# Kernel optimization log

Measured on AMD Instinct MI355X. Metric: run time of the kernel, lower is better.

## Reference

```python
import jax, jax.numpy as jnp
import numpy as np

B, N, HID = 32768, 27, 128
SINKHORN_ITERS = 20
LN_EPS = 1e-5


def _layer_norm(x, g, b):
    mu = jnp.mean(x, axis=-1, keepdims=True)
    var = jnp.mean((x - mu) ** 2, axis=-1, keepdims=True)
    return (x - mu) * jax.lax.rsqrt(var + LN_EPS) * g + b


def setup_inputs() -> dict:
    key = jax.random.key(0)
    ks = jax.random.split(key, 6)
    A = jax.random.uniform(ks[0], (B, N, N), dtype=jnp.float32)
    m = jax.random.normal(ks[1], (B, N), dtype=jnp.float32)
    tau_r = jnp.ones((), dtype=jnp.float32)
    # MLP params: LayerNorm(4) -> Linear(4,128) -> ReLU -> Linear(128,128) -> LayerNorm(128)
    ln1_g = jnp.ones((4,), jnp.float32)
    ln1_b = jnp.zeros((4,), jnp.float32)
    W1 = jax.random.normal(ks[2], (4, HID), dtype=jnp.float32) * 0.1
    b1 = jnp.zeros((HID,), jnp.float32)
    W2 = jax.random.normal(ks[3], (HID, HID), dtype=jnp.float32) * 0.05
    b2 = jnp.zeros((HID,), jnp.float32)
    ln2_g = jnp.ones((HID,), jnp.float32)
    ln2_b = jnp.zeros((HID,), jnp.float32)
    protos = jax.random.normal(ks[4], (N, HID), dtype=jnp.float32) * 0.02
    return {"A": A, "m": m, "tau_r": tau_r, "ln1_g": ln1_g, "ln1_b": ln1_b,
            "W1": W1, "b1": b1, "W2": W2, "b2": b2,
            "ln2_g": ln2_g, "ln2_b": ln2_b, "protos": protos}


def reference(A, m, tau_r, ln1_g, ln1_b, W1, b1, W2, b2, ln2_g, ln2_b, protos):
    # ---- feature build: [log1p(rowsum), top1_offdiag, top2_offdiag, m] ----
    row_sum = jnp.sum(A, axis=-1)                       # (B,N)
    eye = jnp.eye(N, dtype=A.dtype)
    offdiag = A * (1.0 - eye)                           # (B,N,N)
    top2_vals, _ = jax.lax.top_k(offdiag, 2)            # (B,N,2)
    feat = jnp.stack([jnp.log1p(row_sum), top2_vals[..., 0], top2_vals[..., 1], m], axis=-1)  # (B,N,4)
    # ---- MLP: LN -> Linear -> ReLU -> (Dropout=id) -> Linear -> LN ----
    h = _layer_norm(feat, ln1_g, ln1_b)
    h = jax.nn.relu(h @ W1 + b1)
    h = h @ W2 + b2
    H = _layer_norm(h, ln2_g, ln2_b)                    # (B,N,HID)
    # ---- scores vs slot prototypes, transposed, temperature ----
    scores = jnp.einsum('bnh,kh->bnk', H, protos)       # (B,N,N)
    log_alpha = jnp.swapaxes(scores, 1, 2) / tau_r
    # ---- log-domain Sinkhorn, 20 iterations ----
    def body(_, la):
        la = la - jax.nn.logsumexp(la, axis=-1, keepdims=True)
        la = la - jax.nn.logsumexp(la, axis=-2, keepdims=True)
        return la
    log_alpha = jax.lax.fori_loop(0, SINKHORN_ITERS, body, log_alpha)
    return jnp.exp(log_alpha)                           # (B,N,N) soft permutation R_L
```

## Files before the change

kernel.cpp:

```cpp
#include <hip/hip_runtime.h>
#include <math.h>

#define NN 27
#define HID 128
#define SITERS 20
#define H1S 136

typedef float    v4    __attribute__((ext_vector_type(4)));
typedef _Float16 f16x8 __attribute__((ext_vector_type(8)));

__global__ void k0_prep(const float* __restrict__ W2, const float* __restrict__ protos,
                        _Float16* __restrict__ Bsw, _Float16* __restrict__ Asw)
{
    int t0 = blockIdx.x * 256 + threadIdx.x;
    for (int idx = t0; idx < 4*8*64*8; idx += 8*256) {
        int j = idx & 7, l = (idx >> 3) & 63, nt = (idx >> 9) & 7, kt = idx >> 12;
        int k = kt*32 + (l >> 4)*8 + j, n = nt*16 + (l & 15);
        Bsw[idx] = (_Float16)W2[k*HID + n];
    }
    for (int idx = t0; idx < 2*4*64*8; idx += 8*256) {
        int j = idx & 7, l = (idx >> 3) & 63, kt = (idx >> 9) & 3, mt = idx >> 11;
        int k = kt*32 + (l >> 4)*8 + j, mm = mt*16 + (l & 15);
        Asw[idx] = (mm < NN) ? (_Float16)protos[mm*HID + k] : (_Float16)0.0f;
    }
}

__global__ __launch_bounds__(128, 8) void k1_mlp(
    const float* __restrict__ A, const float* __restrict__ m,
    const float* __restrict__ tau_r,
    const float* __restrict__ ln1g, const float* __restrict__ ln1b,
    const float* __restrict__ W1, const float* __restrict__ b1,
    const float* __restrict__ b2,
    const float* __restrict__ ln2g, const float* __restrict__ ln2b,
    const _Float16* __restrict__ Bsw, const _Float16* __restrict__ Asw,
    float* __restrict__ out)
{
    __shared__ __align__(16) _Float16 sBuf[32 * H1S];
    __shared__ __align__(16) float    sFeat[NN*4 + 4];

    float*    sA  = (float*)sBuf;
    _Float16* sH1 = sBuf;
    _Float16* sH  = sBuf;
    float*    sS  = (float*)sBuf;

    const int b   = blockIdx.x;
    const int tid = threadIdx.x;
    const int l = tid & 63, w = tid >> 6;
    const int c = l & 15, g = l >> 4;
    const float* Ab = A + (size_t)b * (NN * NN);

    for (int i = tid; i < NN * NN; i += 128) sA[i] = Ab[i];
    __syncthreads();

    if (tid < NN) {
        const int n = tid;
        float sum = 0.f, m1 = -1e30f, m2 = -1e30f;
        #pragma unroll
        for (int j = 0; j < NN; ++j) {
            float a = sA[n * NN + j];
            sum += a;
            float v = (j == n) ? 0.f : a;
            float nm1 = fmaxf(m1, v);
            m2 = fmaxf(m2, fminf(m1, v));
            m1 = nm1;
        }
        float f0 = log1pf(sum), f1 = m1, f2 = m2, f3 = m[(size_t)b * NN + n];
        float mu = 0.25f * (f0 + f1 + f2 + f3);
        float d0 = f0 - mu, d1 = f1 - mu, d2 = f2 - mu, d3 = f3 - mu;
        float var = 0.25f * (d0*d0 + d1*d1 + d2*d2 + d3*d3);
        float rs  = rsqrtf(var + 1e-5f);
        sFeat[n*4 + 0] = d0 * rs * ln1g[0] + ln1b[0];
        sFeat[n*4 + 1] = d1 * rs * ln1g[1] + ln1b[1];
        sFeat[n*4 + 2] = d2 * rs * ln1g[2] + ln1b[2];
        sFeat[n*4 + 3] = d3 * rs * ln1g[3] + ln1b[3];
    }
    __syncthreads();

    {
        const float w0 = W1[tid], w1 = W1[HID + tid], w2 = W1[2*HID + tid], w3 = W1[3*HID + tid];
        const float bb = b1[tid];
        #pragma unroll 9
        for (int n = 0; n < NN; ++n) {
            v4 f = *(const v4*)&sFeat[n * 4];
            float v = fmaf(f[0], w0, fmaf(f[1], w1, fmaf(f[2], w2, fmaf(f[3], w3, bb))));
            sH1[n * H1S + tid] = (_Float16)fmaxf(v, 0.f);
        }
        #pragma unroll
        for (int n = NN; n < 32; ++n) sH1[n * H1S + tid] = (_Float16)0.f;
    }
    __syncthreads();

    f16x8 af[4];
    #pragma unroll
    for (int kt = 0; kt < 4; ++kt)
        af[kt] = *(const f16x8*)&sH1[(w*16 + c) * H1S + kt*32 + g*8];

    const f16x8* Bv = (const f16x8*)Bsw;

    float s4[4]  = {0.f, 0.f, 0.f, 0.f};
    float ss4[4] = {0.f, 0.f, 0.f, 0.f};
    #pragma unroll 1
    for (int nt = 0; nt < 8; ++nt) {
        v4 a = (v4)(0.f);
        #pragma unroll
        for (int kt = 0; kt < 4; ++kt)
            a = __builtin_amdgcn_mfma_f32_16x16x32_f16(af[kt], Bv[(kt*8 + nt)*64 + l], a, 0, 0, 0);
        float b2v = b2[nt*16 + c];
        #pragma unroll
        for (int r = 0; r < 4; ++r) {
            float v = a[r] + b2v;
            s4[r] += v; ss4[r] += v * v;
        }
    }
    float muv[4], rsv[4];
    #pragma unroll
    for (int r = 0; r < 4; ++r) {
        #pragma unroll
        for (int mask = 1; mask <= 8; mask <<= 1) {
            s4[r]  += __shfl_xor(s4[r],  mask);
            ss4[r] += __shfl_xor(ss4[r], mask);
        }
        float mu  = s4[r] * (1.0f / HID);
        float var = ss4[r] * (1.0f / HID) - mu * mu;
        muv[r] = mu;
        rsv[r] = rsqrtf(var + 1e-5f);
    }

    #pragma unroll 1
    for (int nt = 0; nt < 8; ++nt) {
        v4 a = (v4)(0.f);
        #pragma unroll
        for (int kt = 0; kt < 4; ++kt)
            a = __builtin_amdgcn_mfma_f32_16x16x32_f16(af[kt], Bv[(kt*8 + nt)*64 + l], a, 0, 0, 0);
        int col = nt*16 + c;
        float b2v = b2[col], g2 = ln2g[col], bb = ln2b[col];
        #pragma unroll
        for (int r = 0; r < 4; ++r) {
            float hv = (a[r] + b2v - muv[r]) * rsv[r] * g2 + bb;
            sH[(w*16 + 4*g + r) * H1S + col] = (_Float16)hv;
        }
    }
    __syncthreads();

    v4 acc2[2];
    {
        const f16x8* Av = (const f16x8*)Asw;
        acc2[0] = (v4)(0.f); acc2[1] = (v4)(0.f);
        #pragma unroll
        for (int kt = 0; kt < 4; ++kt) {
            f16x8 pa  = Av[(w*4 + kt)*64 + l];
            f16x8 b0  = *(const f16x8*)&sH[(c)      * H1S + kt*32 + g*8];
            f16x8 b1f = *(const f16x8*)&sH[(16 + c) * H1S + kt*32 + g*8];
            acc2[0] = __builtin_amdgcn_mfma_f32_16x16x32_f16(pa, b0,  acc2[0], 0, 0, 0);
            acc2[1] = __builtin_amdgcn_mfma_f32_16x16x32_f16(pa, b1f, acc2[1], 0, 0, 0);
        }
    }
    __syncthreads();

    {
        const float inv_tau = 1.0f / tau_r[0];
        #pragma unroll
        for (int nt2 = 0; nt2 < 2; ++nt2) {
            int j = nt2*16 + c;
            if (j < NN) {
                #pragma unroll
                for (int r = 0; r < 4; ++r) {
                    int i = w*16 + 4*g + r;
                    if (i < NN) sS[i*28 + j] = __expf(acc2[nt2][r] * inv_tau);
                }
            }
        }
        if (tid < 28) sS[756 + tid] = 1.f;
        if (tid < NN) sS[tid*28 + NN] = 0.f;
    }
    __syncthreads();

    if (w == 0) {
        float* ce = sS + 756;
        const bool act = (l < NN);
        for (int it = 0; it < SITERS; ++it) {
            if (act) {
                float* rp = sS + l * 28;
                float s = 0.f;
                #pragma unroll
                for (int qi = 0; qi < 7; ++qi) {
                    v4 x  = *(const v4*)&rp[qi * 4];
                    v4 cv = *(const v4*)&ce[qi * 4];
                    v4 p  = x * cv;
                    s += p[0] + p[1] + p[2] + p[3];
                }
                float rho = 1.0f / s;
                asm volatile("" ::: "memory");
                #pragma unroll
                for (int qi = 0; qi < 7; ++qi) {
                    v4 x  = *(const v4*)&rp[qi * 4];
                    v4 cv = *(const v4*)&ce[qi * 4];
                    *(v4*)&rp[qi * 4] = x * cv * rho;
                }
            }
            __builtin_amdgcn_wave_barrier();
            if (act) {
                const float* cp = sS + l;
                float s2 = 0.f;
                #pragma unroll
                for (int i2 = 0; i2 < NN; ++i2) s2 += cp[i2 * 28];
                ce[l] = 1.0f / s2;
            }
            __builtin_amdgcn_wave_barrier();
        }
    }
    __syncthreads();

    {
        float* ob = out + (size_t)b * (NN * NN);
        for (int idx = tid; idx < NN * NN; idx += 128) {
            int row = idx / NN, col = idx - row * NN;
            ob[idx] = sS[row * 28 + col] * sS[756 + col];
        }
    }
}

extern "C" void kernel_launch(void* const* d_in, const int* in_sizes, int n_in,
                              void* d_out, int out_size, void* d_ws, size_t ws_size,
                              hipStream_t stream) {
    const float* A      = (const float*)d_in[0];
    const float* m      = (const float*)d_in[1];
    const float* tau_r  = (const float*)d_in[2];
    const float* ln1g   = (const float*)d_in[3];
    const float* ln1b   = (const float*)d_in[4];
    const float* W1     = (const float*)d_in[5];
    const float* b1     = (const float*)d_in[6];
    const float* W2     = (const float*)d_in[7];
    const float* b2     = (const float*)d_in[8];
    const float* ln2g   = (const float*)d_in[9];
    const float* ln2b   = (const float*)d_in[10];
    const float* protos = (const float*)d_in[11];
    float* out = (float*)d_out;

    const int B = in_sizes[0] / (NN * NN);

    _Float16* Bsw = (_Float16*)d_ws;
    _Float16* Asw = (_Float16*)((char*)d_ws + 32768);

    k0_prep<<<8, 256, 0, stream>>>(W2, protos, Bsw, Asw);
    k1_mlp<<<B, 128, 0, stream>>>(A, m, tau_r, ln1g, ln1b, W1, b1, b2,
                                  ln2g, ln2b, Bsw, Asw, out);
}
```

Baseline: 562.4 us.

## Run Sinkhorn iterations in MFMA accumulator registers across both waves

The Sinkhorn normalisation now runs on the MFMA output fragments held in registers by both waves, instead of writing the score matrix to LDS and iterating with a single wave. Row sums use lane shuffles within 16-lane groups. Column sums combine shuffles with a small double-buffered LDS exchange between the two waves, synchronised by a block barrier each iteration. This removes the single-wave serial LDS-bound loop and the final LDS readback, at the cost of 20 block-wide barriers and scattered uncoalesced output stores.

```diff
diff --git a/kernel.cpp b/kernel.cpp
--- a/kernel.cpp
+++ b/kernel.cpp
@@ -38,10 +38,10 @@
     __shared__ __align__(16) _Float16 sBuf[32 * H1S];
     __shared__ __align__(16) float    sFeat[NN*4 + 4];
 
-    float*    sA  = (float*)sBuf;
-    _Float16* sH1 = sBuf;
-    _Float16* sH  = sBuf;
-    float*    sS  = (float*)sBuf;
+    float*    sA   = (float*)sBuf;
+    _Float16* sH1  = sBuf;
+    _Float16* sH   = sBuf;
+    float*    part = (float*)sBuf;
 
     const int b   = blockIdx.x;
     const int tid = threadIdx.x;
@@ -157,65 +157,61 @@
     }
     __syncthreads();
 
+    const int i0 = w*16 + 4*g;
+    const int j1 = 16 + c;
+    float p0[4], p1[4];
     {
         const float inv_tau = 1.0f / tau_r[0];
         #pragma unroll
-        for (int nt2 = 0; nt2 < 2; ++nt2) {
-            int j = nt2*16 + c;
-            if (j < NN) {
-                #pragma unroll
-                for (int r = 0; r < 4; ++r) {
-                    int i = w*16 + 4*g + r;
-                    if (i < NN) sS[i*28 + j] = __expf(acc2[nt2][r] * inv_tau);
-                }
+        for (int r = 0; r < 4; ++r) {
+            bool iok = (i0 + r) < NN;
+            p0[r] = iok ? __expf(acc2[0][r] * inv_tau) : 0.f;
+            p1[r] = (iok && j1 < NN) ? __expf(acc2[1][r] * inv_tau) : 0.f;
+        }
+    }
+
+    for (int it = 0; it < SITERS; ++it) {
+        #pragma unroll
+        for (int r = 0; r < 4; ++r) {
+            float s = p0[r] + p1[r];
+            s += __shfl_xor(s, 1);
+            s += __shfl_xor(s, 2);
+            s += __shfl_xor(s, 4);
+            s += __shfl_xor(s, 8);
+            float rho = ((i0 + r) < NN) ? (1.0f / s) : 0.f;
+            p0[r] *= rho;
+            p1[r] *= rho;
+        }
+        float t0 = (p0[0] + p0[1]) + (p0[2] + p0[3]);
+        float t1 = (p1[0] + p1[1]) + (p1[2] + p1[3]);
+        t0 += __shfl_xor(t0, 16);  t0 += __shfl_xor(t0, 32);
+        t1 += __shfl_xor(t1, 16);  t1 += __shfl_xor(t1, 32);
+        float* pb = part + (it & 1) * 64;
+        if (g == 0) {
+            pb[w*32 + c]      = t0;
+            pb[w*32 + 16 + c] = t1;
+        }
+        __syncthreads();
+        float cs0 = t0 + pb[(w^1)*32 + c];
+        float cs1 = t1 + pb[(w^1)*32 + 16 + c];
+        float rc0 = 1.0f / cs0;
+        float rc1 = (j1 < NN) ? (1.0f / cs1) : 0.f;
+        #pragma unroll
+        for (int r = 0; r < 4; ++r) {
+            p0[r] *= rc0;
+            p1[r] *= rc1;
+        }
+    }
+
+    {
+        float* ob = out + (size_t)b * (NN * NN);
+        #pragma unroll
+        for (int r = 0; r < 4; ++r) {
+            int i = i0 + r;
+            if (i < NN) {
+                ob[i * NN + c] = p0[r];
+                if (j1 < NN) ob[i * NN + j1] = p1[r];
             }
-        }
-        if (tid < 28) sS[756 + tid] = 1.f;
-        if (tid < NN) sS[tid*28 + NN] = 0.f;
-    }
-    __syncthreads();
-
-    if (w == 0) {
-        float* ce = sS + 756;
-        const bool act = (l < NN);
-        for (int it = 0; it < SITERS; ++it) {
-            if (act) {
-                float* rp = sS + l * 28;
-                float s = 0.f;
-                #pragma unroll
-                for (int qi = 0; qi < 7; ++qi) {
-                    v4 x  = *(const v4*)&rp[qi * 4];
-                    v4 cv = *(const v4*)&ce[qi * 4];
-                    v4 p  = x * cv;
-                    s += p[0] + p[1] + p[2] + p[3];
-                }
-                float rho = 1.0f / s;
-                asm volatile("" ::: "memory");
-                #pragma unroll
-                for (int qi = 0; qi < 7; ++qi) {
-                    v4 x  = *(const v4*)&rp[qi * 4];
-                    v4 cv = *(const v4*)&ce[qi * 4];
-                    *(v4*)&rp[qi * 4] = x * cv * rho;
-                }
-            }
-            __builtin_amdgcn_wave_barrier();
-            if (act) {
-                const float* cp = sS + l;
-                float s2 = 0.f;
-                #pragma unroll
-                for (int i2 = 0; i2 < NN; ++i2) s2 += cp[i2 * 28];
-                ce[l] = 1.0f / s2;
-            }
-            __builtin_amdgcn_wave_barrier();
-        }
-    }
-    __syncthreads();
-
-    {
-        float* ob = out + (size_t)b * (NN * NN);
-        for (int idx = tid; idx < NN * NN; idx += 128) {
-            int row = idx / NN, col = idx - row * NN;
-            ob[idx] = sS[row * 28 + col] * sS[756 + col];
         }
     }
 }
```

Result: no change. 568.4 us (+1.1%).
